# Kernel optimization log

Hardware: AMD Instinct MI355X
Metric: run time of the kernel (lower is better)

## Reference

```python
import jax, jax.numpy as jnp
import numpy as np

BETA = 1.0
ALPHA = 0.5


def setup_inputs() -> dict:
    key = jax.random.key(0)
    k1, k2, k3 = jax.random.split(key, 3)
    B, N1, N2 = 512, 256, 32768
    v = jax.random.normal(k1, (B, N1), dtype=jnp.float32)
    mask = jax.random.uniform(k2, (B, N1), dtype=jnp.float32)
    Mem = jax.random.normal(k3, (N2, N1), dtype=jnp.float32)  # kernel [N2, N1] (trailing 1 squeezed)
    return {"v": v, "mask": mask, "Mem": Mem}


def reference(v, mask, Mem):
    # Squared L2 distance d2[i, b] = ||Mem[i] - v[b]||^2, computed without the
    # [N2, N1, B] diff tensor via the expansion ||m||^2 - 2 m.v + ||v||^2.
    m2 = jnp.sum(Mem * Mem, axis=1)            # [N2]
    v2 = jnp.sum(v * v, axis=1)                # [B]
    cross = jnp.einsum('nd,bd->nb', Mem, v)    # [N2, B]
    d2 = m2[:, None] - 2.0 * cross + v2[None, :]
    # Gaussian-kernel weights over the N2 stored patterns (softmax == exp/sum).
    w = jax.nn.softmax(-0.5 * BETA * d2, axis=0)  # [N2, B]
    # update[b] = sum_i w[i,b] * (Mem[i] - v[b]) = (w^T Mem)[b] - v[b]
    update = jnp.einsum('nb,nd->bd', w, Mem) - v   # [B, N1]
    return v + ALPHA * update * mask
```

## Files before the change

### kernel.cpp

```cpp
#include <hip/hip_runtime.h>
#include <hip/hip_bf16.h>
#include <stdint.h>

typedef float  f32x4  __attribute__((ext_vector_type(4)));
typedef float  f32x16 __attribute__((ext_vector_type(16)));
typedef _Float16 half8 __attribute__((ext_vector_type(8)));
typedef unsigned int uint32;

#define N1 256
#define N2T 32768
#define BQ 512
#define KT 32
#define TILE_B 16384

#define RA_OFF 0
#define MT_OFF 32768
#define LDS_BYTES 65536

union H4 { _Float16 h[4]; unsigned short s[4]; uint2 u2; };

#define GLD_LDS(gp, lp) __builtin_amdgcn_global_load_lds( \
    (const __attribute__((address_space(1))) void*)(gp), \
    (__attribute__((address_space(3))) void*)(lp), 16, 0, 0)

__global__ __launch_bounds__(256) void mhn_prep_k(
    const float* __restrict__ Mem, _Float16* __restrict__ MemA,
    _Float16* __restrict__ MemT, float* __restrict__ m2g)
{
  const int t   = blockIdx.x;
  const int tid = threadIdx.x;
  const int a    = tid >> 4;
  const int dblk = tid & 15;
  const int r0i  = 32*t + 2*a;

  const float* p0 = Mem + (size_t)r0i*N1 + dblk*16;
  const float* p1 = p0 + N1;
  float4 x0[4], x1[4];
  #pragma unroll
  for (int i=0;i<4;i++){ x0[i] = *(const float4*)(p0+4*i); x1[i] = *(const float4*)(p1+4*i); }

  float s0=0.f, s1=0.f;
  H4 h0[4], h1[4];
  #pragma unroll
  for (int i=0;i<4;i++){
    s0 += x0[i].x*x0[i].x + x0[i].y*x0[i].y + x0[i].z*x0[i].z + x0[i].w*x0[i].w;
    s1 += x1[i].x*x1[i].x + x1[i].y*x1[i].y + x1[i].z*x1[i].z + x1[i].w*x1[i].w;
    h0[i].h[0]=(_Float16)x0[i].x; h0[i].h[1]=(_Float16)x0[i].y; h0[i].h[2]=(_Float16)x0[i].z; h0[i].h[3]=(_Float16)x0[i].w;
    h1[i].h[0]=(_Float16)x1[i].x; h1[i].h[1]=(_Float16)x1[i].y; h1[i].h[2]=(_Float16)x1[i].z; h1[i].h[3]=(_Float16)x1[i].w;
  }

  char* bA = (char*)MemA + (size_t)t*TILE_B;
  {
    const int e0 = (2*a)&7, e1 = (2*a+1)&7;
    uint4 wv;
    wv.x=h0[0].u2.x; wv.y=h0[0].u2.y; wv.z=h0[1].u2.x; wv.w=h0[1].u2.y;
    *(uint4*)(bA + (2*a)*512   + (((2*dblk  )^e0)<<4)) = wv;
    wv.x=h0[2].u2.x; wv.y=h0[2].u2.y; wv.z=h0[3].u2.x; wv.w=h0[3].u2.y;
    *(uint4*)(bA + (2*a)*512   + (((2*dblk+1)^e0)<<4)) = wv;
    wv.x=h1[0].u2.x; wv.y=h1[0].u2.y; wv.z=h1[1].u2.x; wv.w=h1[1].u2.y;
    *(uint4*)(bA + (2*a+1)*512 + (((2*dblk  )^e1)<<4)) = wv;
    wv.x=h1[2].u2.x; wv.y=h1[2].u2.y; wv.z=h1[3].u2.x; wv.w=h1[3].u2.y;
    *(uint4*)(bA + (2*a+1)*512 + (((2*dblk+1)^e1)<<4)) = wv;
  }

  char* bT = (char*)MemT + (size_t)t*TILE_B;
  #pragma unroll
  for (int i=0;i<4;i++){
    #pragma unroll
    for (int j=0;j<4;j++){
      const int d = dblk*16 + 4*i + j;
      const uint32 pk = (uint32)h0[i].s[j] | ((uint32)h1[i].s[j] << 16);
      *(uint32*)(bT + d*64 + ((((a>>2) ^ ((d>>1)&3)))<<4) + ((a&3)<<2)) = pk;
    }
  }

  s0 += __shfl_xor(s0,1); s0 += __shfl_xor(s0,2); s0 += __shfl_xor(s0,4); s0 += __shfl_xor(s0,8);
  s1 += __shfl_xor(s1,1); s1 += __shfl_xor(s1,2); s1 += __shfl_xor(s1,4); s1 += __shfl_xor(s1,8);
  if (dblk == 0){ m2g[r0i] = -0.5f*s0; m2g[r0i+1] = -0.5f*s1; }
}

__global__ __launch_bounds__(256, 2) void mhn_flash_k(
    const _Float16* __restrict__ MemA, const _Float16* __restrict__ MemT,
    const float* __restrict__ m2g, const float* __restrict__ v,
    __hip_bfloat16* __restrict__ Opart, float* __restrict__ mpart,
    float* __restrict__ lpart, int CK, int nt)
{
  __shared__ __align__(16) char lds[LDS_BYTES];

  const int tid = threadIdx.x;
  const int w   = tid >> 6;
  const int l   = tid & 63;
  const int row = l & 31;
  const int hi  = l >> 5;

  const int nwg = gridDim.x;
  const int bid = blockIdx.x;
  const int s_  = (bid & 7) * (nwg >> 3) + (bid >> 3);
  const int c   = s_ >> 2;
  const int qb  = s_ & 3;

  auto dma = [&](int tt, int bw){
    const size_t off = (size_t)(c*(CK>>5) + tt)*TILE_B + w*4096 + l*16;
    const char* gA = (const char*)MemA + off;
    const char* gT = (const char*)MemT + off;
    char* dA = lds + RA_OFF + bw*TILE_B + w*4096 + l*16;
    char* dT = lds + MT_OFF + bw*TILE_B + w*4096 + l*16;
    #pragma unroll
    for (int i=0;i<4;i++){
      GLD_LDS(gA + i*1024, dA + i*1024);
      GLD_LDS(gT + i*1024, dT + i*1024);
    }
  };

  dma(0, 0);

  half8 v8[16];
  const int q0 = qb*128 + w*32;
  {
    const float* vp = v + (size_t)(q0 + row)*N1 + 8*hi;
    #pragma unroll
    for (int s=0;s<16;s++){
      const float4 a = *(const float4*)(vp + 16*s);
      const float4 b = *(const float4*)(vp + 16*s + 4);
      half8 hv;
      hv[0]=(_Float16)a.x; hv[1]=(_Float16)a.y; hv[2]=(_Float16)a.z; hv[3]=(_Float16)a.w;
      hv[4]=(_Float16)b.x; hv[5]=(_Float16)b.y; hv[6]=(_Float16)b.z; hv[7]=(_Float16)b.w;
      v8[s]=hv;
    }
  }

  float mrun = -INFINITY, lrun = 0.f;
  f32x16 oacc[8];
  #pragma unroll
  for (int b=0;b<8;b++) oacc[b] = (f32x16)(0.f);

  const int e7 = row & 7;
  const uint32 qkB = (uint32)(row*512 + ((hi ^ (e7 & 1)) << 4) + ((e7 >> 1) << 5));
  const int sd = (row >> 1) & 3;
  const uint32 pvB = (uint32)(row*64 + ((hi ^ (sd & 1)) << 4) + ((sd >> 1) << 5));

  __syncthreads();

  for (int tt=0; tt<nt; ++tt){
    const int buf = tt & 1;
    const bool pf = (tt+1 < nt);
    if (pf) dma(tt+1, buf^1);

    const float* m2p = m2g + c*CK + tt*KT;
    f32x4 m2v[4];
    #pragma unroll
    for (int b=0;b<4;b++) m2v[b] = *(const f32x4*)(m2p + 8*b + 4*hi);

    const char* ra = lds + RA_OFF + buf*TILE_B;
    f32x16 S = (f32x16)(0.f);
    #pragma unroll
    for (int s=0;s<16;s++){
      const half8 a = *(const half8*)(ra + (qkB ^ (uint32)(s<<5)));
      S = __builtin_amdgcn_mfma_f32_32x32x16_f16(a, v8[s], S, 0,0,0);
    }

    float p[16];
    #pragma unroll
    for (int r=0;r<16;r++) p[r] = S[r] + m2v[r>>2][r&3];

    float tm = p[0];
    #pragma unroll
    for (int r=1;r<16;r++) tm = fmaxf(tm, p[r]);
    tm = fmaxf(tm, __shfl_xor(tm, 32));
    if (__any(tm > mrun + 8.0f)){
      const float nm = fmaxf(mrun, tm);
      const float sc = __expf(mrun - nm);
      lrun *= sc; mrun = nm;
      #pragma unroll
      for (int b=0;b<8;b++) oacc[b] *= sc;
    }
    #pragma unroll
    for (int r=0;r<16;r++) p[r] = __expf(p[r] - mrun);
    float ps = 0.f;
    #pragma unroll
    for (int r=0;r<16;r++) ps += p[r];
    ps += __shfl_xor(ps, 32); lrun += ps;

    uint32 D[8];
    #pragma unroll
    for (int i=0;i<8;i++){
      union { __fp16 h2 __attribute__((ext_vector_type(2))); uint32 u; } cv;
      cv.h2 = __builtin_amdgcn_cvt_pkrtz(p[2*i], p[2*i+1]);
      D[i] = cv.u;
    }
    uint32 wq[8];
    {
      const uint32 tD0 = (uint32)__shfl_xor((int)D[0], 32);
      const uint32 tD1 = (uint32)__shfl_xor((int)D[1], 32);
      const uint32 tD2 = (uint32)__shfl_xor((int)D[2], 32);
      const uint32 tD3 = (uint32)__shfl_xor((int)D[3], 32);
      const uint32 tD4 = (uint32)__shfl_xor((int)D[4], 32);
      const uint32 tD5 = (uint32)__shfl_xor((int)D[5], 32);
      const uint32 tD6 = (uint32)__shfl_xor((int)D[6], 32);
      const uint32 tD7 = (uint32)__shfl_xor((int)D[7], 32);
      const bool lo = (hi == 0);
      wq[0] = lo ? D[0] : tD2;  wq[1] = lo ? D[1] : tD3;
      wq[2] = lo ? tD0 : D[2];  wq[3] = lo ? tD1 : D[3];
      wq[4] = lo ? D[4] : tD6;  wq[5] = lo ? D[5] : tD7;
      wq[6] = lo ? tD4 : D[6];  wq[7] = lo ? tD5 : D[7];
    }
    union { uint32 u[4]; half8 h; } pb1, pb2;
    pb1.u[0]=wq[0]; pb1.u[1]=wq[1]; pb1.u[2]=wq[2]; pb1.u[3]=wq[3];
    pb2.u[0]=wq[4]; pb2.u[1]=wq[5]; pb2.u[2]=wq[6]; pb2.u[3]=wq[7];

    const char* mtb = lds + MT_OFF + buf*TILE_B;
    const char* a1 = (const char*)(mtb + pvB);
    const char* a2 = (const char*)(mtb + (pvB ^ 32u));
    #pragma unroll
    for (int b=0;b<8;b++){
      const half8 A1 = *(const half8*)(a1 + b*2048);
      oacc[b] = __builtin_amdgcn_mfma_f32_32x32x16_f16(A1, pb1.h, oacc[b], 0,0,0);
      const half8 A2 = *(const half8*)(a2 + b*2048);
      oacc[b] = __builtin_amdgcn_mfma_f32_32x32x16_f16(A2, pb2.h, oacc[b], 0,0,0);
    }

    __syncthreads();
  }

  {
    __hip_bfloat16* Op = Opart + (size_t)c*N1*BQ + (q0 + row);
    #pragma unroll
    for (int b=0;b<8;b++){
      #pragma unroll
      for (int r=0;r<16;r++){
        const int d = 32*b + (r&3) + 8*(r>>2) + 4*hi;
        Op[(size_t)d*BQ] = __float2bfloat16(oacc[b][r]);
      }
    }
    if (hi == 0){
      mpart[(size_t)c*BQ + q0 + row] = mrun;
      lpart[(size_t)c*BQ + q0 + row] = lrun;
    }
  }
}

__global__ __launch_bounds__(128) void mhn_wprep_k(
    const float* __restrict__ mpart, const float* __restrict__ lpart,
    float* __restrict__ W, float* __restrict__ invL, int nchunk)
{
  __shared__ float sred[2];
  const int q = blockIdx.x;
  const int c = threadIdx.x;
  const int l = c & 63, wv = c >> 6;

  const float m = (c < nchunk) ? mpart[(size_t)c*BQ + q] : -INFINITY;
  const float lv = (c < nchunk) ? lpart[(size_t)c*BQ + q] : 0.f;

  float r = m;
  r = fmaxf(r, __shfl_xor(r,1));  r = fmaxf(r, __shfl_xor(r,2));
  r = fmaxf(r, __shfl_xor(r,4));  r = fmaxf(r, __shfl_xor(r,8));
  r = fmaxf(r, __shfl_xor(r,16)); r = fmaxf(r, __shfl_xor(r,32));
  if (l == 0) sred[wv] = r;
  __syncthreads();
  const float M = fmaxf(sred[0], sred[1]);
  __syncthreads();

  const float e = __expf(m - M);
  float s = lv * e;
  s += __shfl_xor(s,1);  s += __shfl_xor(s,2);
  s += __shfl_xor(s,4);  s += __shfl_xor(s,8);
  s += __shfl_xor(s,16); s += __shfl_xor(s,32);
  if (l == 0) sred[wv] = s;
  __syncthreads();

  if (c < nchunk) W[(size_t)c*BQ + q] = e;
  if (c == 0) invL[q] = 1.0f / (sred[0] + sred[1]);
}

__global__ __launch_bounds__(256) void mhn_wsum_k(
    const float* __restrict__ v, const float* __restrict__ mask,
    const __hip_bfloat16* __restrict__ Opart, const float* __restrict__ W,
    const float* __restrict__ invL, float* __restrict__ out, int nchunk)
{
  const int g = blockIdx.x*256 + threadIdx.x;
  const int q = g & (BQ-1);
  const int d = g >> 9;

  const __hip_bfloat16* op = Opart + (size_t)d*BQ + q;
  const float* wp = W + q;
  float acc = 0.f;
  #pragma unroll 8
  for (int c2=0; c2<nchunk; c2++){
    acc += __bfloat162float(op[(size_t)c2*N1*BQ]) * wp[(size_t)c2*BQ];
  }
  const float vv = v[(size_t)q*N1 + d], mk = mask[(size_t)q*N1 + d];
  out[(size_t)q*N1 + d] = vv + 0.5f*(acc*invL[q] - vv)*mk;
}

extern "C" void kernel_launch(void* const* d_in, const int* in_sizes, int n_in,
                              void* d_out, int out_size, void* d_ws, size_t ws_size,
                              hipStream_t stream)
{
  (void)in_sizes; (void)n_in; (void)out_size;
  const float* v    = (const float*)d_in[0];
  const float* mask = (const float*)d_in[1];
  const float* Mem  = (const float*)d_in[2];
  float* out = (float*)d_out;

  const size_t fixedB   = (size_t)N2T*N1*2*2 + (size_t)N2T*4 + (size_t)BQ*4;
  const size_t perChunk = (size_t)BQ*N1*2 + (size_t)BQ*12;
  int nchunk = 128;
  while (nchunk > 4 && fixedB + (size_t)nchunk*perChunk > ws_size) nchunk >>= 1;

  char* wsb = (char*)d_ws;
  _Float16* MemA = (_Float16*)wsb;
  _Float16* MemT = (_Float16*)(wsb + (size_t)N2T*N1*2);
  float*    m2g  = (float*)(wsb + (size_t)N2T*N1*4);
  float*    invL = (float*)(wsb + (size_t)N2T*N1*4 + (size_t)N2T*4);
  char* pb = wsb + fixedB;
  __hip_bfloat16* Opart = (__hip_bfloat16*)pb;
  float* mpart = (float*)(pb + (size_t)nchunk*BQ*N1*2);
  float* lpart = mpart + (size_t)nchunk*BQ;
  float* W     = lpart + (size_t)nchunk*BQ;

  const int CK = N2T / nchunk;
  const int nt = CK / KT;

  mhn_prep_k<<<dim3(N2T/KT), dim3(256), 0, stream>>>(Mem, MemA, MemT, m2g);
  mhn_flash_k<<<dim3(4*nchunk), dim3(256), 0, stream>>>(MemA, MemT, m2g, v, Opart, mpart, lpart, CK, nt);
  mhn_wprep_k<<<dim3(BQ), dim3(128), 0, stream>>>(mpart, lpart, W, invL, nchunk);
  mhn_wsum_k<<<dim3((N1*BQ)/256), dim3(256), 0, stream>>>(v, mask, Opart, W, invL, out, nchunk);
}
```

Before: 69.42 us.

## Read PV operand directly from global in fragment order, halve LDS staging

Prep kernel now writes both fp16 copies of Mem in MFMA fragment order, so per-lane loads are contiguous with no XOR swizzle. The flash kernel stages only the QK operand tile through LDS via global_load_lds, halving LDS use. The PV operand is loaded directly from global memory per wave with one-step register prefetch. The softmax row-sum is deferred after the PV MFMAs. This trades LDS traffic and footprint for redundant per-wave global/L2 reads and exposed global latency in the inner loop.

New measurement: 70.49 us. Within noise of the previous version (+1.5%).

```diff
diff --git a/kernel.cpp b/kernel.cpp
--- a/kernel.cpp
+++ b/kernel.cpp
@@ -13,9 +13,7 @@
 #define KT 32
 #define TILE_B 16384
 
-#define RA_OFF 0
-#define MT_OFF 32768
-#define LDS_BYTES 65536
+#define LDS_BYTES 32768
 
 union H4 { _Float16 h[4]; unsigned short s[4]; uint2 u2; };
 
@@ -24,8 +22,8 @@
     (__attribute__((address_space(3))) void*)(lp), 16, 0, 0)
 
 __global__ __launch_bounds__(256) void mhn_prep_k(
-    const float* __restrict__ Mem, _Float16* __restrict__ MemA,
-    _Float16* __restrict__ MemT, float* __restrict__ m2g)
+    const float* __restrict__ Mem, _Float16* __restrict__ rowF,
+    _Float16* __restrict__ memF, float* __restrict__ m2g)
 {
   const int t   = blockIdx.x;
   const int tid = threadIdx.x;
@@ -49,28 +47,31 @@
     h1[i].h[0]=(_Float16)x1[i].x; h1[i].h[1]=(_Float16)x1[i].y; h1[i].h[2]=(_Float16)x1[i].z; h1[i].h[3]=(_Float16)x1[i].w;
   }
 
-  char* bA = (char*)MemA + (size_t)t*TILE_B;
   {
-    const int e0 = (2*a)&7, e1 = (2*a+1)&7;
-    uint4 wv;
-    wv.x=h0[0].u2.x; wv.y=h0[0].u2.y; wv.z=h0[1].u2.x; wv.w=h0[1].u2.y;
-    *(uint4*)(bA + (2*a)*512   + (((2*dblk  )^e0)<<4)) = wv;
-    wv.x=h0[2].u2.x; wv.y=h0[2].u2.y; wv.z=h0[3].u2.x; wv.w=h0[3].u2.y;
-    *(uint4*)(bA + (2*a)*512   + (((2*dblk+1)^e0)<<4)) = wv;
-    wv.x=h1[0].u2.x; wv.y=h1[0].u2.y; wv.z=h1[1].u2.x; wv.w=h1[1].u2.y;
-    *(uint4*)(bA + (2*a+1)*512 + (((2*dblk  )^e1)<<4)) = wv;
-    wv.x=h1[2].u2.x; wv.y=h1[2].u2.y; wv.z=h1[3].u2.x; wv.w=h1[3].u2.y;
-    *(uint4*)(bA + (2*a+1)*512 + (((2*dblk+1)^e1)<<4)) = wv;
-  }
-
-  char* bT = (char*)MemT + (size_t)t*TILE_B;
-  #pragma unroll
-  for (int i=0;i<4;i++){
-    #pragma unroll
-    for (int j=0;j<4;j++){
-      const int d = dblk*16 + 4*i + j;
-      const uint32 pk = (uint32)h0[i].s[j] | ((uint32)h1[i].s[j] << 16);
-      *(uint32*)(bT + d*64 + ((((a>>2) ^ ((d>>1)&3)))<<4) + ((a&3)<<2)) = pk;
+    char* bF = (char*)rowF + (size_t)t*TILE_B + dblk*1024;
+    #pragma unroll
+    for (int hi=0; hi<2; hi++){
+      uint4 wa, wb;
+      wa.x = h0[2*hi].u2.x;   wa.y = h0[2*hi].u2.y;
+      wa.z = h0[2*hi+1].u2.x; wa.w = h0[2*hi+1].u2.y;
+      wb.x = h1[2*hi].u2.x;   wb.y = h1[2*hi].u2.y;
+      wb.z = h1[2*hi+1].u2.x; wb.w = h1[2*hi+1].u2.y;
+      *(uint4*)(bF + (2*a  )*16 + hi*512) = wa;
+      *(uint4*)(bF + (2*a+1)*16 + hi*512) = wb;
+    }
+  }
+
+  {
+    char* bM = (char*)memF + (size_t)t*TILE_B
+             + (size_t)(2*(dblk>>1) + (a>>3))*1024
+             + (size_t)((dblk&1)*16 + 32*((a>>2)&1))*16
+             + (size_t)(a&3)*4;
+    #pragma unroll
+    for (int i=0;i<4;i++){
+      #pragma unroll
+      for (int j=0;j<4;j++){
+        *(uint32*)(bM + (4*i+j)*16) = (uint32)h0[i].s[j] | ((uint32)h1[i].s[j] << 16);
+      }
     }
   }
 
@@ -80,7 +81,7 @@
 }
 
 __global__ __launch_bounds__(256, 2) void mhn_flash_k(
-    const _Float16* __restrict__ MemA, const _Float16* __restrict__ MemT,
+    const _Float16* __restrict__ rowF, const _Float16* __restrict__ memF,
     const float* __restrict__ m2g, const float* __restrict__ v,
     __hip_bfloat16* __restrict__ Opart, float* __restrict__ mpart,
     float* __restrict__ lpart, int CK, int nt)
@@ -98,21 +99,15 @@
   const int s_  = (bid & 7) * (nwg >> 3) + (bid >> 3);
   const int c   = s_ >> 2;
   const int qb  = s_ & 3;
-
-  auto dma = [&](int tt, int bw){
-    const size_t off = (size_t)(c*(CK>>5) + tt)*TILE_B + w*4096 + l*16;
-    const char* gA = (const char*)MemA + off;
-    const char* gT = (const char*)MemT + off;
-    char* dA = lds + RA_OFF + bw*TILE_B + w*4096 + l*16;
-    char* dT = lds + MT_OFF + bw*TILE_B + w*4096 + l*16;
-    #pragma unroll
-    for (int i=0;i<4;i++){
-      GLD_LDS(gA + i*1024, dA + i*1024);
-      GLD_LDS(gT + i*1024, dT + i*1024);
-    }
-  };
-
-  dma(0, 0);
+  const int tpc = CK >> 5;
+
+  const uint32 dmaL = (uint32)(w*4096 + l*16);
+  const char* gR = (const char*)rowF + (size_t)(c*tpc)*TILE_B + dmaL;
+  char* const dR0 = lds + dmaL;
+
+  #pragma unroll
+  for (int i=0;i<4;i++) GLD_LDS(gR + i*1024, dR0 + i*1024);
+  gR += TILE_B;
 
   half8 v8[16];
   const int q0 = qb*128 + w*32;
@@ -134,28 +129,30 @@
   #pragma unroll
   for (int b=0;b<8;b++) oacc[b] = (f32x16)(0.f);
 
-  const int e7 = row & 7;
-  const uint32 qkB = (uint32)(row*512 + ((hi ^ (e7 & 1)) << 4) + ((e7 >> 1) << 5));
-  const int sd = (row >> 1) & 3;
-  const uint32 pvB = (uint32)(row*64 + ((hi ^ (sd & 1)) << 4) + ((sd >> 1) << 5));
+  const float* m2p = m2g + c*CK + 4*hi;
+  const char* gT = (const char*)memF + (size_t)(c*tpc)*TILE_B + (uint32)l*16;
 
   __syncthreads();
 
   for (int tt=0; tt<nt; ++tt){
-    const int buf = tt & 1;
+    const uint32 bufO = (uint32)(tt & 1)*TILE_B;
     const bool pf = (tt+1 < nt);
-    if (pf) dma(tt+1, buf^1);
-
-    const float* m2p = m2g + c*CK + tt*KT;
+    if (pf){
+      char* dR = dR0 + (bufO ^ TILE_B);
+      #pragma unroll
+      for (int i=0;i<4;i++) GLD_LDS(gR + i*1024, dR + i*1024);
+      gR += TILE_B;
+    }
+
     f32x4 m2v[4];
     #pragma unroll
-    for (int b=0;b<4;b++) m2v[b] = *(const f32x4*)(m2p + 8*b + 4*hi);
-
-    const char* ra = lds + RA_OFF + buf*TILE_B;
+    for (int b=0;b<4;b++) m2v[b] = *(const f32x4*)(m2p + 8*b);
+
+    const char* ra = lds + bufO + (uint32)l*16;
     f32x16 S = (f32x16)(0.f);
     #pragma unroll
     for (int s=0;s<16;s++){
-      const half8 a = *(const half8*)(ra + (qkB ^ (uint32)(s<<5)));
+      const half8 a = *(const half8*)(ra + s*1024);
       S = __builtin_amdgcn_mfma_f32_32x32x16_f16(a, v8[s], S, 0,0,0);
     }
 
@@ -176,10 +173,6 @@
     }
     #pragma unroll
     for (int r=0;r<16;r++) p[r] = __expf(p[r] - mrun);
-    float ps = 0.f;
-    #pragma unroll
-    for (int r=0;r<16;r++) ps += p[r];
-    ps += __shfl_xor(ps, 32); lrun += ps;
 
     uint32 D[8];
     #pragma unroll
@@ -208,17 +201,27 @@
     pb1.u[0]=wq[0]; pb1.u[1]=wq[1]; pb1.u[2]=wq[2]; pb1.u[3]=wq[3];
     pb2.u[0]=wq[4]; pb2.u[1]=wq[5]; pb2.u[2]=wq[6]; pb2.u[3]=wq[7];
 
-    const char* mtb = lds + MT_OFF + buf*TILE_B;
-    const char* a1 = (const char*)(mtb + pvB);
-    const char* a2 = (const char*)(mtb + (pvB ^ 32u));
+    half8 A1 = *(const half8*)(gT);
+    half8 A2 = *(const half8*)(gT + 1024);
     #pragma unroll
     for (int b=0;b<8;b++){
-      const half8 A1 = *(const half8*)(a1 + b*2048);
+      half8 nA1, nA2;
+      if (b < 7){
+        nA1 = *(const half8*)(gT + (2*b+2)*1024);
+        nA2 = *(const half8*)(gT + (2*b+3)*1024);
+      }
       oacc[b] = __builtin_amdgcn_mfma_f32_32x32x16_f16(A1, pb1.h, oacc[b], 0,0,0);
-      const half8 A2 = *(const half8*)(a2 + b*2048);
       oacc[b] = __builtin_amdgcn_mfma_f32_32x32x16_f16(A2, pb2.h, oacc[b], 0,0,0);
-    }
-
+      if (b < 7){ A1 = nA1; A2 = nA2; }
+    }
+    gT += TILE_B;
+
+    float ps = 0.f;
+    #pragma unroll
+    for (int r=0;r<16;r++) ps += p[r];
+    ps += __shfl_xor(ps, 32); lrun += ps;
+
+    m2p += KT;
     __syncthreads();
   }
 
@@ -308,8 +311,8 @@
   while (nchunk > 4 && fixedB + (size_t)nchunk*perChunk > ws_size) nchunk >>= 1;
 
   char* wsb = (char*)d_ws;
-  _Float16* MemA = (_Float16*)wsb;
-  _Float16* MemT = (_Float16*)(wsb + (size_t)N2T*N1*2);
+  _Float16* rowF = (_Float16*)wsb;
+  _Float16* memF = (_Float16*)(wsb + (size_t)N2T*N1*2);
   float*    m2g  = (float*)(wsb + (size_t)N2T*N1*4);
   float*    invL = (float*)(wsb + (size_t)N2T*N1*4 + (size_t)N2T*4);
   char* pb = wsb + fixedB;
@@ -321,8 +324,8 @@
   const int CK = N2T / nchunk;
   const int nt = CK / KT;
 
-  mhn_prep_k<<<dim3(N2T/KT), dim3(256), 0, stream>>>(Mem, MemA, MemT, m2g);
-  mhn_flash_k<<<dim3(4*nchunk), dim3(256), 0, stream>>>(MemA, MemT, m2g, v, Opart, mpart, lpart, CK, nt);
+  mhn_prep_k<<<dim3(N2T/KT), dim3(256), 0, stream>>>(Mem, rowF, memF, m2g);
+  mhn_flash_k<<<dim3(4*nchunk), dim3(256), 0, stream>>>(rowF, memF, m2g, v, Opart, mpart, lpart, CK, nt);
   mhn_wprep_k<<<dim3(BQ), dim3(128), 0, stream>>>(mpart, lpart, W, invL, nchunk);
   mhn_wsum_k<<<dim3((N1*BQ)/256), dim3(256), 0, stream>>>(v, mask, Opart, W, invL, out, nchunk);
 }
```
